# Kernel optimization log

Measured on AMD Instinct MI355X. Metric: run time of the kernel, lower is better.

The kernel has to match this reference:

```python
import jax, jax.numpy as jnp
import numpy as np

GROUP = 8          # weight_group_size
QMAX = 7.0         # 2**(4-1)-1, narrow-range symmetric int4
EPS = 1e-8


def quant_dequant(w):
    """Per-group (size 8, along in_features) symmetric int4 quant-dequant.
    w: [out, in] -> dequantized [out, in]."""
    O, I = w.shape
    wg = w.reshape(O, I // GROUP, GROUP)
    scale = jnp.max(jnp.abs(wg), axis=-1, keepdims=True) / QMAX  # [O, I/G, 1]
    scale = jnp.maximum(scale, EPS)
    q = jnp.clip(jnp.round(wg / scale), -QMAX, QMAX)
    return (q * scale).reshape(O, I)


def setup_inputs() -> dict:
    key = jax.random.key(0)
    kx, kw, kb = jax.random.split(key, 3)
    tokens, din, dout = 8192, 4096, 4096
    x = jax.random.normal(kx, (tokens, din), dtype=jnp.float32)
    weight = jax.random.normal(kw, (dout, din), dtype=jnp.float32) * 0.02
    bias = jax.random.normal(kb, (dout,), dtype=jnp.float32) * 0.01
    return {"x": x, "weight": weight, "bias": bias}


def reference(x, weight, bias):
    w_deq = quant_dequant(weight)                 # [out, in]
    return jnp.dot(x, w_deq.T) + bias             # [tokens, out]
```

## Files before the change

kernel.cpp:

```cpp
#include <hip/hip_runtime.h>
#include <hip/hip_bf16.h>
#include <stdint.h>

typedef __attribute__((ext_vector_type(8))) __bf16 bf16x8;
typedef __attribute__((ext_vector_type(4))) float f32x4;
typedef __attribute__((ext_vector_type(8))) unsigned short ushort8;

typedef const void __attribute__((address_space(1))) gv_t;
typedef void __attribute__((address_space(3))) lv_t;

#define GL16(g, l) __builtin_amdgcn_global_load_lds((gv_t*)(g), (lv_t*)(l), 16, 0, 0)

__device__ __forceinline__ unsigned short f2bf(float f) {
    unsigned int u = __float_as_uint(f);
    u += 0x7fffu + ((u >> 16) & 1u);
    return (unsigned short)(u >> 16);
}

__global__ void __launch_bounds__(256) qdq_weight(const float* __restrict__ w,
                                                  unsigned short* __restrict__ wb,
                                                  int n_groups) {
    int g = blockIdx.x * 256 + threadIdx.x;
    if (g >= n_groups) return;
    const float4* p = (const float4*)w + (size_t)g * 2;
    float4 v0 = p[0], v1 = p[1];
    float t[8] = {v0.x, v0.y, v0.z, v0.w, v1.x, v1.y, v1.z, v1.w};
    float amax = 0.0f;
#pragma unroll
    for (int j = 0; j < 8; ++j) amax = fmaxf(amax, fabsf(t[j]));
    float scale = fmaxf(amax / 7.0f, 1e-8f);
    ushort8 o;
#pragma unroll
    for (int j = 0; j < 8; ++j) {
        float q = rintf(t[j] / scale);
        q = fminf(fmaxf(q, -7.0f), 7.0f);
        o[j] = f2bf(q * scale);
    }
    *((ushort8*)wb + g) = o;
}

__global__ void __launch_bounds__(256) cvt_bf16(const float* __restrict__ x,
                                                unsigned short* __restrict__ xb,
                                                int n8) {
    int i = blockIdx.x * 256 + threadIdx.x;
    if (i >= n8) return;
    const float4* p = (const float4*)x + (size_t)i * 2;
    float4 v0 = p[0], v1 = p[1];
    ushort8 o;
    o[0] = f2bf(v0.x); o[1] = f2bf(v0.y); o[2] = f2bf(v0.z); o[3] = f2bf(v0.w);
    o[4] = f2bf(v1.x); o[5] = f2bf(v1.y); o[6] = f2bf(v1.z); o[7] = f2bf(v1.w);
    *((ushort8*)xb + i) = o;
}

#define BM 256
#define BN 256
#define BK 64

#define BAR_()   asm volatile("s_barrier" ::: "memory")
#define VM0_()   asm volatile("s_waitcnt vmcnt(0)" ::: "memory")

#define STAGE_T(sdst, gsrc, b, kk)                                             \
    {                                                                          \
        _Pragma("unroll")                                                      \
        for (int rr = 0; rr < 8; ++rr)                                         \
            GL16(gsrc + (size_t)(rr * 32 + srow) * K + (kk) + schunk,          \
                 &sdst[b][(rr * 32 + w * 8) * BK]);                            \
    }

__global__ void __launch_bounds__(256, 1)
gemmBW(const unsigned short* __restrict__ A,
       const unsigned short* __restrict__ B,
       const float* __restrict__ bias,
       float* __restrict__ C,
       int M, int N, int K) {
    __shared__ unsigned short sA[2][BM * BK];
    __shared__ unsigned short sB[2][BN * BK];

    const int t  = threadIdx.x;
    const int w  = t >> 6;
    const int ln = t & 63;
    const int lr = ln & 15;
    const int lk = ln >> 4;
    const int wr = w >> 1;
    const int wc = w & 1;

    const int nbn = N / BN;
    const int bid = blockIdx.x;
    const int swz = ((int)gridDim.x & 7) ? bid
                  : ((bid & 7) * ((int)gridDim.x >> 3) + (bid >> 3));
    const int m0 = (swz / nbn) * BM;
    const int n0 = (swz % nbn) * BN;

    const unsigned short* gA = A + (size_t)m0 * K;
    const unsigned short* gB = B + (size_t)n0 * K;

    const int srow   = t >> 3;
    const int schunk = (((t & 7) ^ (srow & 7)) << 3);

    const int sw = (lr & 7) << 3;
    const int e0 = (lk * 8) ^ sw;
    const int e1 = (32 + lk * 8) ^ sw;

    f32x4 acc[8][8];
#pragma unroll
    for (int i = 0; i < 8; ++i)
#pragma unroll
        for (int j = 0; j < 8; ++j)
            acc[i][j] = (f32x4)(0.0f);

    const int NT = K / BK;

    STAGE_T(sA, gA, 0, 0);
    STAGE_T(sB, gB, 0, 0);
    VM0_();
    BAR_();

    for (int tt = 0; tt < NT; ++tt) {
        const int cur = tt & 1;
        const int nxt = cur ^ 1;

        if (tt + 1 < NT) {
            const int kk = (tt + 1) * BK;
            STAGE_T(sA, gA, nxt, kk);
            STAGE_T(sB, gB, nxt, kk);
        }

        bf16x8 af[8][2];
#pragma unroll
        for (int mi = 0; mi < 8; ++mi) {
            const int s_ = (wr * 128 + mi * 16 + lr) * BK;
            af[mi][0] = *(const bf16x8*)&sA[cur][s_ + e0];
            af[mi][1] = *(const bf16x8*)&sA[cur][s_ + e1];
        }

#pragma unroll
        for (int ni = 0; ni < 8; ++ni) {
            const int s_ = (wc * 128 + ni * 16 + lr) * BK;
            bf16x8 b0 = *(const bf16x8*)&sB[cur][s_ + e0];
            bf16x8 b1 = *(const bf16x8*)&sB[cur][s_ + e1];
#pragma unroll
            for (int mi = 0; mi < 8; ++mi) {
                acc[mi][ni] = __builtin_amdgcn_mfma_f32_16x16x32_bf16(
                    af[mi][0], b0, acc[mi][ni], 0, 0, 0);
                acc[mi][ni] = __builtin_amdgcn_mfma_f32_16x16x32_bf16(
                    af[mi][1], b1, acc[mi][ni], 0, 0, 0);
            }
        }

        VM0_();
        BAR_();
    }

#pragma unroll
    for (int ni = 0; ni < 8; ++ni) {
        const int n = n0 + wc * 128 + ni * 16 + lr;
        const float bv = bias[n];
#pragma unroll
        for (int mi = 0; mi < 8; ++mi) {
            const int m = m0 + wr * 128 + mi * 16 + lk * 4;
            f32x4 v = acc[mi][ni];
            C[(size_t)(m + 0) * N + n] = v[0] + bv;
            C[(size_t)(m + 1) * N + n] = v[1] + bv;
            C[(size_t)(m + 2) * N + n] = v[2] + bv;
            C[(size_t)(m + 3) * N + n] = v[3] + bv;
        }
    }
}

extern "C" void kernel_launch(void* const* d_in, const int* in_sizes, int n_in,
                              void* d_out, int out_size, void* d_ws, size_t ws_size,
                              hipStream_t stream) {
    const float* x    = (const float*)d_in[0];
    const float* wgt  = (const float*)d_in[1];
    const float* bias = (const float*)d_in[2];
    float* out        = (float*)d_out;

    const int dout = in_sizes[2];
    const int din  = in_sizes[1] / dout;
    const int M    = in_sizes[0] / din;
    const int N    = dout, K = din;

    unsigned short* xb = (unsigned short*)d_ws;
    unsigned short* wb = xb + (size_t)M * K;

    const int ng_w = (N * K) / 8;
    qdq_weight<<<(ng_w + 255) / 256, 256, 0, stream>>>(wgt, wb, ng_w);

    const int n8_x = (M * K) / 8;
    cvt_bf16<<<(n8_x + 255) / 256, 256, 0, stream>>>(x, xb, n8_x);

    const int nwg = (M / BM) * (N / BN);
    gemmBW<<<nwg, 256, 0, stream>>>(xb, wb, bias, out, M, N, K);
}
```

Before: 352.7 us.

## Load B fragments directly to registers, stage only A in LDS with 8 waves

The GEMM now runs 512 threads (8 waves, 2x4 layout) with BK=32. Only the A tile is staged in LDS. Each wave loads its own B fragments straight from global memory into registers, double-buffered across k-steps. Partial vmcnt waits, sched barriers and setprio around the MFMA blocks are meant to overlap the loads with compute and cut LDS traffic and footprint. The cost is that B fragments are no longer shared through LDS, so global and L2 traffic for B rises, and BK is halved so barriers are more frequent.

```diff
diff --git a/kernel.cpp b/kernel.cpp
--- a/kernel.cpp
+++ b/kernel.cpp
@@ -54,35 +54,56 @@
 
 #define BM 256
 #define BN 256
-#define BK 64
-
-#define BAR_()   asm volatile("s_barrier" ::: "memory")
-#define VM0_()   asm volatile("s_waitcnt vmcnt(0)" ::: "memory")
-
-#define STAGE_T(sdst, gsrc, b, kk)                                             \
+#define BK 32
+
+#define BAR_() asm volatile("s_barrier" ::: "memory")
+#define VM4_() asm volatile("s_waitcnt vmcnt(4)" ::: "memory")
+#define SB_()  __builtin_amdgcn_sched_barrier(0)
+
+#define STAGE_A2(b, kk)                                                        \
     {                                                                          \
+        GL16(gA + (size_t)(srow) * K + (kk) + schunk,                          \
+             &sA[b][(w * 16) * BK]);                                           \
+        GL16(gA + (size_t)(128 + srow) * K + (kk) + schunk,                    \
+             &sA[b][(128 + w * 16) * BK]);                                     \
+    }
+
+#define LOADB(dst, kk)                                                         \
+    _Pragma("unroll")                                                          \
+    for (int ni = 0; ni < 4; ++ni)                                             \
+        dst[ni] = *(const bf16x8*)(gBn[ni] + (kk));
+
+#define READ_A(b)                                                              \
+    _Pragma("unroll")                                                          \
+    for (int mi = 0; mi < 8; ++mi)                                             \
+        af[mi] = *(const bf16x8*)&sA[b][(wr * 128 + mi * 16 + lr) * BK + ce];
+
+#define MFMA_T(BF)                                                             \
+    __builtin_amdgcn_s_setprio(1);                                             \
+    _Pragma("unroll")                                                          \
+    for (int ni = 0; ni < 4; ++ni)                                             \
         _Pragma("unroll")                                                      \
-        for (int rr = 0; rr < 8; ++rr)                                         \
-            GL16(gsrc + (size_t)(rr * 32 + srow) * K + (kk) + schunk,          \
-                 &sdst[b][(rr * 32 + w * 8) * BK]);                            \
-    }
-
-__global__ void __launch_bounds__(256, 1)
-gemmBW(const unsigned short* __restrict__ A,
+        for (int mi = 0; mi < 8; ++mi)                                         \
+            acc[mi][ni] = __builtin_amdgcn_mfma_f32_16x16x32_bf16(             \
+                af[mi], BF[ni], acc[mi][ni], 0, 0, 0);                         \
+    __builtin_amdgcn_s_setprio(0);
+
+__global__ void __launch_bounds__(512, 1)
+gemmBD(const unsigned short* __restrict__ A,
        const unsigned short* __restrict__ B,
        const float* __restrict__ bias,
        float* __restrict__ C,
        int M, int N, int K) {
     __shared__ unsigned short sA[2][BM * BK];
-    __shared__ unsigned short sB[2][BN * BK];
 
     const int t  = threadIdx.x;
     const int w  = t >> 6;
     const int ln = t & 63;
     const int lr = ln & 15;
     const int lk = ln >> 4;
-    const int wr = w >> 1;
-    const int wc = w & 1;
+    const int wr = w >> 2;
+    const int wc = w & 3;
+    const int bcol = wc * 64;
 
     const int nbn = N / BN;
     const int bid = blockIdx.x;
@@ -92,68 +113,64 @@
     const int n0 = (swz % nbn) * BN;
 
     const unsigned short* gA = A + (size_t)m0 * K;
-    const unsigned short* gB = B + (size_t)n0 * K;
-
-    const int srow   = t >> 3;
-    const int schunk = (((t & 7) ^ (srow & 7)) << 3);
-
-    const int sw = (lr & 7) << 3;
-    const int e0 = (lk * 8) ^ sw;
-    const int e1 = (32 + lk * 8) ^ sw;
-
-    f32x4 acc[8][8];
+
+    const unsigned short* gBn[4];
+#pragma unroll
+    for (int ni = 0; ni < 4; ++ni)
+        gBn[ni] = B + (size_t)(n0 + bcol + ni * 16 + lr) * K + lk * 8;
+
+    const int srow   = t >> 2;
+    const int schunk = (((t & 3) ^ ((t >> 4) & 3)) << 3);
+
+    const int ce = ((lk ^ ((lr >> 2) & 3)) << 3);
+
+    f32x4 acc[8][4];
 #pragma unroll
     for (int i = 0; i < 8; ++i)
 #pragma unroll
-        for (int j = 0; j < 8; ++j)
+        for (int j = 0; j < 4; ++j)
             acc[i][j] = (f32x4)(0.0f);
 
+    bf16x8 af[8], b_a[4], b_b[4];
+
     const int NT = K / BK;
 
-    STAGE_T(sA, gA, 0, 0);
-    STAGE_T(sB, gB, 0, 0);
-    VM0_();
+    STAGE_A2(0, 0);
+    SB_();
+    LOADB(b_a, 0);
+    SB_();
+    VM4_();
     BAR_();
 
-    for (int tt = 0; tt < NT; ++tt) {
-        const int cur = tt & 1;
-        const int nxt = cur ^ 1;
-
-        if (tt + 1 < NT) {
-            const int kk = (tt + 1) * BK;
-            STAGE_T(sA, gA, nxt, kk);
-            STAGE_T(sB, gB, nxt, kk);
+    for (int tt = 0; tt < NT; tt += 2) {
+        const int k1 = (tt + 1) * BK;
+        const int k2 = (tt + 2) * BK;
+        const bool st2 = (tt + 2 < NT);
+
+        STAGE_A2(1, k1);
+        SB_();
+        LOADB(b_b, k1);
+        SB_();
+        READ_A(0);
+        MFMA_T(b_a);
+        VM4_();
+        BAR_();
+
+        if (st2) {
+            STAGE_A2(0, k2);
+            SB_();
+            LOADB(b_a, k2);
+            SB_();
         }
-
-        bf16x8 af[8][2];
-#pragma unroll
-        for (int mi = 0; mi < 8; ++mi) {
-            const int s_ = (wr * 128 + mi * 16 + lr) * BK;
-            af[mi][0] = *(const bf16x8*)&sA[cur][s_ + e0];
-            af[mi][1] = *(const bf16x8*)&sA[cur][s_ + e1];
-        }
-
-#pragma unroll
-        for (int ni = 0; ni < 8; ++ni) {
-            const int s_ = (wc * 128 + ni * 16 + lr) * BK;
-            bf16x8 b0 = *(const bf16x8*)&sB[cur][s_ + e0];
-            bf16x8 b1 = *(const bf16x8*)&sB[cur][s_ + e1];
-#pragma unroll
-            for (int mi = 0; mi < 8; ++mi) {
-                acc[mi][ni] = __builtin_amdgcn_mfma_f32_16x16x32_bf16(
-                    af[mi][0], b0, acc[mi][ni], 0, 0, 0);
-                acc[mi][ni] = __builtin_amdgcn_mfma_f32_16x16x32_bf16(
-                    af[mi][1], b1, acc[mi][ni], 0, 0, 0);
-            }
-        }
-
-        VM0_();
+        READ_A(1);
+        MFMA_T(b_b);
+        VM4_();
         BAR_();
     }
 
 #pragma unroll
-    for (int ni = 0; ni < 8; ++ni) {
-        const int n = n0 + wc * 128 + ni * 16 + lr;
+    for (int ni = 0; ni < 4; ++ni) {
+        const int n = n0 + bcol + ni * 16 + lr;
         const float bv = bias[n];
 #pragma unroll
         for (int mi = 0; mi < 8; ++mi) {
@@ -190,5 +207,5 @@
     cvt_bf16<<<(n8_x + 255) / 256, 256, 0, stream>>>(x, xb, n8_x);
 
     const int nwg = (M / BM) * (N / BN);
-    gemmBW<<<nwg, 256, 0, stream>>>(xb, wb, bias, out, M, N, K);
-}
+    gemmBD<<<nwg, 512, 0, stream>>>(xb, wb, bias, out, M, N, K);
+}
```

Measured after the change: 418.7 us. 1.19x slower.

## Rework GEMM to 512-thread blocks with split LDS halves and merge prep kernels

Applied to the files above, without the earlier changes.

Merges the weight quant-dequant and activation bf16 conversion into one launch. Reorganises the bf16 GEMM from 4 waves per 256x256 tile to 8 waves, each computing a 128x64 sub-tile, which halves per-wave accumulator registers and allows two blocks per CU. LDS is split into half-tiles with new staging and read patterns, and all fragment reads for both k-steps are issued before the MFMAs, which run under raised wave priority. The risks are more LDS traffic per MFMA from the smaller per-wave tile and LDS capacity limits on the requested occupancy.

```diff
diff --git a/kernel.cpp b/kernel.cpp
--- a/kernel.cpp
+++ b/kernel.cpp
@@ -17,39 +17,39 @@
     return (unsigned short)(u >> 16);
 }
 
-__global__ void __launch_bounds__(256) qdq_weight(const float* __restrict__ w,
-                                                  unsigned short* __restrict__ wb,
-                                                  int n_groups) {
-    int g = blockIdx.x * 256 + threadIdx.x;
-    if (g >= n_groups) return;
-    const float4* p = (const float4*)w + (size_t)g * 2;
-    float4 v0 = p[0], v1 = p[1];
-    float t[8] = {v0.x, v0.y, v0.z, v0.w, v1.x, v1.y, v1.z, v1.w};
-    float amax = 0.0f;
-#pragma unroll
-    for (int j = 0; j < 8; ++j) amax = fmaxf(amax, fabsf(t[j]));
-    float scale = fmaxf(amax / 7.0f, 1e-8f);
-    ushort8 o;
-#pragma unroll
-    for (int j = 0; j < 8; ++j) {
-        float q = rintf(t[j] / scale);
-        q = fminf(fmaxf(q, -7.0f), 7.0f);
-        o[j] = f2bf(q * scale);
-    }
-    *((ushort8*)wb + g) = o;
-}
-
-__global__ void __launch_bounds__(256) cvt_bf16(const float* __restrict__ x,
-                                                unsigned short* __restrict__ xb,
-                                                int n8) {
-    int i = blockIdx.x * 256 + threadIdx.x;
-    if (i >= n8) return;
-    const float4* p = (const float4*)x + (size_t)i * 2;
-    float4 v0 = p[0], v1 = p[1];
-    ushort8 o;
-    o[0] = f2bf(v0.x); o[1] = f2bf(v0.y); o[2] = f2bf(v0.z); o[3] = f2bf(v0.w);
-    o[4] = f2bf(v1.x); o[5] = f2bf(v1.y); o[6] = f2bf(v1.z); o[7] = f2bf(v1.w);
-    *((ushort8*)xb + i) = o;
+__global__ void __launch_bounds__(256) prep(const float* __restrict__ w,
+                                            const float* __restrict__ x,
+                                            unsigned short* __restrict__ wb,
+                                            unsigned short* __restrict__ xb,
+                                            int ng_w, int n8_x) {
+    int id = blockIdx.x * 256 + threadIdx.x;
+    if (id < ng_w) {
+        const float4* p = (const float4*)w + (size_t)id * 2;
+        float4 v0 = p[0], v1 = p[1];
+        float t[8] = {v0.x, v0.y, v0.z, v0.w, v1.x, v1.y, v1.z, v1.w};
+        float amax = 0.0f;
+#pragma unroll
+        for (int j = 0; j < 8; ++j) amax = fmaxf(amax, fabsf(t[j]));
+        float scale = fmaxf(amax / 7.0f, 1e-8f);
+        ushort8 o;
+#pragma unroll
+        for (int j = 0; j < 8; ++j) {
+            float q = rintf(t[j] / scale);
+            q = fminf(fmaxf(q, -7.0f), 7.0f);
+            o[j] = f2bf(q * scale);
+        }
+        *((ushort8*)wb + id) = o;
+    } else {
+        int i = id - ng_w;
+        if (i < n8_x) {
+            const float4* p = (const float4*)x + (size_t)i * 2;
+            float4 v0 = p[0], v1 = p[1];
+            ushort8 o;
+            o[0] = f2bf(v0.x); o[1] = f2bf(v0.y); o[2] = f2bf(v0.z); o[3] = f2bf(v0.w);
+            o[4] = f2bf(v1.x); o[5] = f2bf(v1.y); o[6] = f2bf(v1.z); o[7] = f2bf(v1.w);
+            *((ushort8*)xb + i) = o;
+        }
+    }
 }
 
 #define BM 256
@@ -58,31 +58,66 @@
 
 #define BAR_()   asm volatile("s_barrier" ::: "memory")
 #define VM0_()   asm volatile("s_waitcnt vmcnt(0)" ::: "memory")
-
-#define STAGE_T(sdst, gsrc, b, kk)                                             \
+#define LGKM0_() asm volatile("s_waitcnt lgkmcnt(0)" ::: "memory")
+
+#define STAGE_A(b, h, kk)                                                      \
     {                                                                          \
+        GL16(gA + (size_t)((h) * 64 + srow) * K + (kk) + schunk,               \
+             &sA[b][h][0] + sldso);                                            \
+        GL16(gA + (size_t)((h) * 64 + 128 + srow) * K + (kk) + schunk,         \
+             &sA[b][h][64 * BK] + sldso);                                      \
+    }
+#define STAGE_B(b, h, kk)                                                      \
+    {                                                                          \
+        GL16(gB + (size_t)((h) * 32 + brow) * K + (kk) + schunk,               \
+             &sB[b][h][0] + sldso);                                            \
+        GL16(gB + (size_t)((h) * 32 + 128 + brow) * K + (kk) + schunk,         \
+             &sB[b][h][64 * BK] + sldso);                                      \
+    }
+
+#define READ_A_KS(dst, b, h, ks)                                               \
+    _Pragma("unroll")                                                          \
+    for (int mi = 0; mi < 4; ++mi)                                             \
+        dst[mi] = *(const bf16x8*)&sA[b][h][(wr * 64 + mi * 16 + lr) * BK + eks[ks]];
+#define READ_B_KS(dst, b, h, ks)                                               \
+    _Pragma("unroll")                                                          \
+    for (int ni = 0; ni < 2; ++ni)                                             \
+        dst[ni] = *(const bf16x8*)&sB[b][h][(bcol + ni * 16 + lr) * BK + eks[ks]];
+
+#define MFMA_KS(AL, AH, BL, BH)                                                \
+    __builtin_amdgcn_s_setprio(1);                                             \
+    _Pragma("unroll")                                                          \
+    for (int mi = 0; mi < 4; ++mi)                                             \
         _Pragma("unroll")                                                      \
-        for (int rr = 0; rr < 8; ++rr)                                         \
-            GL16(gsrc + (size_t)(rr * 32 + srow) * K + (kk) + schunk,          \
-                 &sdst[b][(rr * 32 + w * 8) * BK]);                            \
-    }
-
-__global__ void __launch_bounds__(256, 1)
-gemmBW(const unsigned short* __restrict__ A,
-       const unsigned short* __restrict__ B,
-       const float* __restrict__ bias,
-       float* __restrict__ C,
-       int M, int N, int K) {
-    __shared__ unsigned short sA[2][BM * BK];
-    __shared__ unsigned short sB[2][BN * BK];
+        for (int ni = 0; ni < 2; ++ni) {                                       \
+            acc[mi][ni]     = __builtin_amdgcn_mfma_f32_16x16x32_bf16(         \
+                AL[mi], BL[ni], acc[mi][ni], 0, 0, 0);                         \
+            acc[mi][2 + ni] = __builtin_amdgcn_mfma_f32_16x16x32_bf16(         \
+                AL[mi], BH[ni], acc[mi][2 + ni], 0, 0, 0);                     \
+            acc[4 + mi][ni] = __builtin_amdgcn_mfma_f32_16x16x32_bf16(         \
+                AH[mi], BL[ni], acc[4 + mi][ni], 0, 0, 0);                     \
+            acc[4 + mi][2 + ni] = __builtin_amdgcn_mfma_f32_16x16x32_bf16(     \
+                AH[mi], BH[ni], acc[4 + mi][2 + ni], 0, 0, 0);                 \
+        }                                                                      \
+    __builtin_amdgcn_s_setprio(0);
+
+__global__ void __launch_bounds__(512, 2)
+gemm256(const unsigned short* __restrict__ A,
+        const unsigned short* __restrict__ B,
+        const float* __restrict__ bias,
+        float* __restrict__ C,
+        int M, int N, int K) {
+    __shared__ unsigned short sA[2][2][128 * BK];
+    __shared__ unsigned short sB[2][2][128 * BK];
 
     const int t  = threadIdx.x;
     const int w  = t >> 6;
     const int ln = t & 63;
     const int lr = ln & 15;
     const int lk = ln >> 4;
-    const int wr = w >> 1;
-    const int wc = w & 1;
+    const int wr = w >> 2;
+    const int wc = w & 3;
+    const int bcol = (wc >> 1) * 64 + (wc & 1) * 32;
 
     const int nbn = N / BN;
     const int bid = blockIdx.x;
@@ -95,25 +130,31 @@
     const unsigned short* gB = B + (size_t)n0 * K;
 
     const int srow   = t >> 3;
+    const int brow   = (srow & 31) + ((srow >> 5) << 6);
     const int schunk = (((t & 7) ^ (srow & 7)) << 3);
-
-    const int sw = (lr & 7) << 3;
-    const int e0 = (lk * 8) ^ sw;
-    const int e1 = (32 + lk * 8) ^ sw;
-
-    f32x4 acc[8][8];
+    const int sldso  = (w * 8) * BK;
+
+    int eks[2];
+#pragma unroll
+    for (int ks = 0; ks < 2; ++ks)
+        eks[ks] = (((ks * 4 + lk) ^ (lr & 7)) << 3);
+
+    f32x4 acc[8][4];
 #pragma unroll
     for (int i = 0; i < 8; ++i)
 #pragma unroll
-        for (int j = 0; j < 8; ++j)
+        for (int j = 0; j < 4; ++j)
             acc[i][j] = (f32x4)(0.0f);
 
     const int NT = K / BK;
 
-    STAGE_T(sA, gA, 0, 0);
-    STAGE_T(sB, gB, 0, 0);
+    STAGE_A(0, 0, 0); STAGE_A(0, 1, 0);
+    STAGE_B(0, 0, 0); STAGE_B(0, 1, 0);
     VM0_();
     BAR_();
+
+    bf16x8 al[4], ah[4], bl[2], bh[2];
+    bf16x8 al1[4], ah1[4], bl1[2], bh1[2];
 
     for (int tt = 0; tt < NT; ++tt) {
         const int cur = tt & 1;
@@ -121,44 +162,31 @@
 
         if (tt + 1 < NT) {
             const int kk = (tt + 1) * BK;
-            STAGE_T(sA, gA, nxt, kk);
-            STAGE_T(sB, gB, nxt, kk);
-        }
-
-        bf16x8 af[8][2];
-#pragma unroll
-        for (int mi = 0; mi < 8; ++mi) {
-            const int s_ = (wr * 128 + mi * 16 + lr) * BK;
-            af[mi][0] = *(const bf16x8*)&sA[cur][s_ + e0];
-            af[mi][1] = *(const bf16x8*)&sA[cur][s_ + e1];
-        }
-
-#pragma unroll
-        for (int ni = 0; ni < 8; ++ni) {
-            const int s_ = (wc * 128 + ni * 16 + lr) * BK;
-            bf16x8 b0 = *(const bf16x8*)&sB[cur][s_ + e0];
-            bf16x8 b1 = *(const bf16x8*)&sB[cur][s_ + e1];
-#pragma unroll
-            for (int mi = 0; mi < 8; ++mi) {
-                acc[mi][ni] = __builtin_amdgcn_mfma_f32_16x16x32_bf16(
-                    af[mi][0], b0, acc[mi][ni], 0, 0, 0);
-                acc[mi][ni] = __builtin_amdgcn_mfma_f32_16x16x32_bf16(
-                    af[mi][1], b1, acc[mi][ni], 0, 0, 0);
-            }
-        }
-
+            STAGE_A(nxt, 0, kk); STAGE_A(nxt, 1, kk);
+            STAGE_B(nxt, 0, kk); STAGE_B(nxt, 1, kk);
+        }
+
+        READ_A_KS(al, cur, 0, 0); READ_A_KS(ah, cur, 1, 0);
+        READ_B_KS(bl, cur, 0, 0); READ_B_KS(bh, cur, 1, 0);
+        READ_A_KS(al1, cur, 0, 1); READ_A_KS(ah1, cur, 1, 1);
+        READ_B_KS(bl1, cur, 0, 1); READ_B_KS(bh1, cur, 1, 1);
+
+        MFMA_KS(al, ah, bl, bh);
+        MFMA_KS(al1, ah1, bl1, bh1);
+
+        LGKM0_();
         VM0_();
         BAR_();
     }
 
 #pragma unroll
-    for (int ni = 0; ni < 8; ++ni) {
-        const int n = n0 + wc * 128 + ni * 16 + lr;
+    for (int j = 0; j < 4; ++j) {
+        const int n = n0 + wc * 64 + (j >> 1) * 32 + (j & 1) * 16 + lr;
         const float bv = bias[n];
 #pragma unroll
-        for (int mi = 0; mi < 8; ++mi) {
-            const int m = m0 + wr * 128 + mi * 16 + lk * 4;
-            f32x4 v = acc[mi][ni];
+        for (int i = 0; i < 8; ++i) {
+            const int m = m0 + wr * 128 + (i >> 2) * 64 + (i & 3) * 16 + lk * 4;
+            f32x4 v = acc[i][j];
             C[(size_t)(m + 0) * N + n] = v[0] + bv;
             C[(size_t)(m + 1) * N + n] = v[1] + bv;
             C[(size_t)(m + 2) * N + n] = v[2] + bv;
@@ -184,11 +212,9 @@
     unsigned short* wb = xb + (size_t)M * K;
 
     const int ng_w = (N * K) / 8;
-    qdq_weight<<<(ng_w + 255) / 256, 256, 0, stream>>>(wgt, wb, ng_w);
-
     const int n8_x = (M * K) / 8;
-    cvt_bf16<<<(n8_x + 255) / 256, 256, 0, stream>>>(x, xb, n8_x);
+    prep<<<(ng_w + n8_x + 255) / 256, 256, 0, stream>>>(wgt, x, wb, xb, ng_w, n8_x);
 
     const int nwg = (M / BM) * (N / BN);
-    gemmBW<<<nwg, 256, 0, stream>>>(xb, wb, bias, out, M, N, K);
-}
+    gemm256<<<nwg, 512, 0, stream>>>(xb, wb, bias, out, M, N, K);
+}
```

Measured after the change: 310.0 us. 12.1% less time.
